# Performance work log

Hardware: AMD Instinct MI355X
Metric: run time of the kernel (lower is better)

Reference implementation:

```python
import jax, jax.numpy as jnp
import numpy as np


def setup_inputs() -> dict:
    key = jax.random.key(0)
    k0, k1, k2, k3 = jax.random.split(key, 4)
    B, T, D, F, E = 4, 2048, 512, 1024, 8
    x = jax.random.normal(k0, (B, T, D), dtype=jnp.float32)
    # router weight is zero-init in the original; use small random values so top-k
    router_w = 0.02 * jax.random.normal(k1, (E, D), dtype=jnp.float32)
    router_b = jnp.zeros((E,), dtype=jnp.float32)
    w_gate_up = 0.02 * jax.random.normal(k2, (E, D, 2 * F), dtype=jnp.float32)
    w_down = 0.02 * jax.random.normal(k3, (E, F, D), dtype=jnp.float32)
    return {"x": x, "router_w": router_w, "router_b": router_b,
            "w_gate_up": w_gate_up, "w_down": w_down, "top_k": 2}


def reference(x, router_w, router_b, w_gate_up, w_down, top_k):
    B, T, D = x.shape
    E = router_w.shape[0]
    x_flat = x.reshape(-1, D)                      # [N, D]
    N = x_flat.shape[0]

    # router: softmax over experts, top-k, renormalize
    logits = x_flat @ router_w.T + router_b       # [N, E]
    probs = jax.nn.softmax(logits, axis=-1)
    top_w, top_idx = jax.lax.top_k(probs, top_k)  # [N, k]
    top_w = top_w / jnp.sum(top_w, axis=-1, keepdims=True)

    # scatter renormalized weights into a dense [N, E] combine matrix
    combine = jnp.zeros((N, E), dtype=x.dtype).at[
        jnp.arange(N)[:, None], top_idx].add(top_w)

    # per-expert SwiGLU; combine weights zero out non-selected experts, giving
    # math identical to the sort/gather/scatter dispatch in the original
    out = jnp.zeros_like(x_flat)
    for e in range(E):  # fixed small expert count, not a data-dim loop
        gate_up = x_flat @ w_gate_up[e]           # [N, 2F]
        gate, up = jnp.split(gate_up, 2, axis=-1)
        h = jax.nn.silu(gate) * up                # [N, F]
        out = out + combine[:, e:e + 1] * (h @ w_down[e])
    return out.reshape(B, T, D)
```

## Files before the change

### kernel.cpp

```cpp
#include <hip/hip_runtime.h>
#include <stdint.h>

#define N_TOK 8192
#define D_DIM 512
#define F_DIM 1024
#define E_NUM 8
#define M_SLOTS (N_TOK * 2)

typedef __bf16 bf16x8 __attribute__((ext_vector_type(8)));
typedef float f32x4 __attribute__((ext_vector_type(4)));

__device__ __forceinline__ ushort f2b(float f) {
    union { float f; unsigned u; } v; v.f = f;
    unsigned r = v.u + 0x7fffu + ((v.u >> 16) & 1u);
    return (ushort)(r >> 16);
}
__device__ __forceinline__ float b2f(ushort u) {
    union { unsigned i; float f; } v; v.i = ((unsigned)u) << 16; return v.f;
}
__device__ __forceinline__ void gload16(const void* g, void* l) {
    __builtin_amdgcn_global_load_lds(
        (const __attribute__((address_space(1))) unsigned int*)g,
        (__attribute__((address_space(3))) unsigned int*)l, 16, 0, 0);
}

__global__ void init_k(int* cnt) {
    if (threadIdx.x < 16) cnt[threadIdx.x] = 0;
}

__global__ __launch_bounds__(256) void transpose_k(const float* __restrict__ in,
                                                   ushort* __restrict__ out,
                                                   int R, int C) {
    __shared__ ushort tile[64][66];
    int e = blockIdx.z;
    const float* src = in + (size_t)e * R * C;
    ushort* dst = out + (size_t)e * R * C;
    int c0 = blockIdx.x * 64, r0 = blockIdx.y * 64;
    for (int i = threadIdx.x; i < 64 * 64; i += 256) {
        int r = i >> 6, c = i & 63;
        tile[r][c] = f2b(src[(size_t)(r0 + r) * C + c0 + c]);
    }
    __syncthreads();
    for (int i = threadIdx.x; i < 64 * 64; i += 256) {
        int c = i >> 6, r = i & 63;
        dst[(size_t)(c0 + c) * R + r0 + r] = tile[r][c];
    }
}

__global__ __launch_bounds__(256) void logits_k(const float* __restrict__ x,
                                                const float* __restrict__ rw,
                                                const float* __restrict__ rb,
                                                ushort* __restrict__ x_bf,
                                                int* __restrict__ tok_e,
                                                float* __restrict__ tok_w) {
    int lane = threadIdx.x & 63, wv = threadIdx.x >> 6;
    int t = blockIdx.x * 4 + wv;
    float4 xa = *(const float4*)(x + (size_t)t * D_DIM + lane * 8);
    float4 xb = *(const float4*)(x + (size_t)t * D_DIM + lane * 8 + 4);
    ushort u[8] = {f2b(xa.x), f2b(xa.y), f2b(xa.z), f2b(xa.w),
                   f2b(xb.x), f2b(xb.y), f2b(xb.z), f2b(xb.w)};
    *(uint4*)(x_bf + (size_t)t * D_DIM + lane * 8) = *(const uint4*)u;

    float acc[E_NUM];
#pragma unroll
    for (int e = 0; e < E_NUM; ++e) {
        float4 wa = *(const float4*)(rw + (size_t)e * D_DIM + lane * 8);
        float4 wb = *(const float4*)(rw + (size_t)e * D_DIM + lane * 8 + 4);
        float s = xa.x * wa.x + xa.y * wa.y + xa.z * wa.z + xa.w * wa.w +
                  xb.x * wb.x + xb.y * wb.y + xb.z * wb.z + xb.w * wb.w;
#pragma unroll
        for (int o = 32; o > 0; o >>= 1) s += __shfl_xor(s, o, 64);
        acc[e] = s;
    }
    if (lane == 0) {
        float l[E_NUM];
#pragma unroll
        for (int e = 0; e < E_NUM; ++e) l[e] = acc[e] + rb[e];
        int e0 = 0;
#pragma unroll
        for (int e = 1; e < E_NUM; ++e) if (l[e] > l[e0]) e0 = e;
        int e1 = (e0 == 0) ? 1 : 0;
#pragma unroll
        for (int e = 0; e < E_NUM; ++e) if (e != e0 && l[e] > l[e1]) e1 = e;
        float p1 = __expf(l[e1] - l[e0]);
        float w0 = 1.f / (1.f + p1), w1 = p1 / (1.f + p1);
        tok_e[2 * t] = e0;  tok_e[2 * t + 1] = e1;
        tok_w[2 * t] = w0;  tok_w[2 * t + 1] = w1;
    }
}

__global__ __launch_bounds__(256) void assign_k(const int* __restrict__ tok_e,
                                                int* __restrict__ cnt,
                                                int* __restrict__ rank) {
    __shared__ int lcnt[E_NUM], lbase[E_NUM];
    int tid = threadIdx.x;
    int i = blockIdx.x * 256 + tid;
    if (tid < E_NUM) lcnt[tid] = 0;
    __syncthreads();
    int e = tok_e[i];
    int intra = atomicAdd(&lcnt[e], 1);
    __syncthreads();
    if (tid < E_NUM) lbase[tid] = atomicAdd(&cnt[tid], lcnt[tid]);
    __syncthreads();
    rank[i] = lbase[e] + intra;
}

__global__ void prefix_k(const int* __restrict__ cnt, int* __restrict__ ebase) {
    if (threadIdx.x == 0) {
        int s = 0;
        for (int e = 0; e < E_NUM; ++e) { ebase[e] = s; s += cnt[e]; }
        ebase[E_NUM] = s;
    }
}

__global__ __launch_bounds__(256) void scatter_k(const int* __restrict__ tok_e,
                                                 const int* __restrict__ rank,
                                                 const int* __restrict__ ebase,
                                                 int* __restrict__ row_token,
                                                 int* __restrict__ tok_pos) {
    int i = blockIdx.x * 256 + threadIdx.x;
    int pos = ebase[tok_e[i]] + rank[i];
    row_token[pos] = i >> 1;
    tok_pos[i] = pos;
}

__global__ __launch_bounds__(256, 4) void gemm1_k(const ushort* __restrict__ x,
                                                  const ushort* __restrict__ wgu_t,
                                                  const int* __restrict__ ebase,
                                                  const int* __restrict__ row_token,
                                                  ushort* __restrict__ h) {
    int e = blockIdx.z;
    int base = ebase[e];
    int cnt = ebase[e + 1] - base;
    int tile0 = blockIdx.y * 128;
    if (tile0 >= cnt) return;
    int c0 = blockIdx.x * 64;

    __shared__ ushort smem[128 * 32 + 128 * 32];
    ushort* lds_a = smem;
    ushort* lds_b = smem + 128 * 32;

    int tid = threadIdx.x;
    int lane = tid & 63, wv = tid >> 6;
    int wr = wv >> 1, wc = wv & 1;

    const ushort* asrc[2];
#pragma unroll
    for (int i = 0; i < 2; ++i) {
        int c = tid + i * 256;
        int r = tile0 + (c >> 2);
        r = (r < cnt) ? r : (cnt - 1);
        int tok = row_token[base + r];
        asrc[i] = x + (size_t)tok * D_DIM + (c & 3) * 8;
    }
    const ushort* bsrc[2];
#pragma unroll
    for (int i = 0; i < 2; ++i) {
        int c = tid + i * 256;
        int brow = c >> 2;
        int gc = (brow < 64) ? (c0 + brow) : (F_DIM + c0 + brow - 64);
        bsrc[i] = wgu_t + ((size_t)e * (2 * F_DIM) + gc) * D_DIM + (c & 3) * 8;
    }

    f32x4 accg[4][2], accu[4][2];
#pragma unroll
    for (int a = 0; a < 4; ++a)
#pragma unroll
        for (int b = 0; b < 2; ++b) {
            accg[a][b] = (f32x4){0.f, 0.f, 0.f, 0.f};
            accu[a][b] = (f32x4){0.f, 0.f, 0.f, 0.f};
        }

    for (int k0 = 0; k0 < D_DIM; k0 += 32) {
        __syncthreads();
#pragma unroll
        for (int i = 0; i < 2; ++i) {
            int c = tid + i * 256;
            gload16(asrc[i] + k0, lds_a + (size_t)c * 8);
            gload16(bsrc[i] + k0, lds_b + (size_t)c * 8);
        }
        __syncthreads();

        int q = lane >> 4, m = lane & 15;
        bf16x8 af[4], bg[2], bu[2];
#pragma unroll
        for (int mt = 0; mt < 4; ++mt)
            af[mt] = *(const bf16x8*)(lds_a + (wr * 64 + mt * 16 + m) * 32 + q * 8);
#pragma unroll
        for (int nt = 0; nt < 2; ++nt) {
            bg[nt] = *(const bf16x8*)(lds_b + (wc * 32 + nt * 16 + m) * 32 + q * 8);
            bu[nt] = *(const bf16x8*)(lds_b + (64 + wc * 32 + nt * 16 + m) * 32 + q * 8);
        }
#pragma unroll
        for (int mt = 0; mt < 4; ++mt)
#pragma unroll
            for (int nt = 0; nt < 2; ++nt) {
                accg[mt][nt] = __builtin_amdgcn_mfma_f32_16x16x32_bf16(af[mt], bg[nt], accg[mt][nt], 0, 0, 0);
                accu[mt][nt] = __builtin_amdgcn_mfma_f32_16x16x32_bf16(af[mt], bu[nt], accu[mt][nt], 0, 0, 0);
            }
    }

    ushort* stg = smem;
    int q = lane >> 4, col = lane & 15;
    __syncthreads();
#pragma unroll
    for (int mt = 0; mt < 4; ++mt) {
#pragma unroll
        for (int nt = 0; nt < 2; ++nt) {
            int sc = wc * 32 + nt * 16 + col;
#pragma unroll
            for (int r4 = 0; r4 < 4; ++r4) {
                int sr = wr * 16 + q * 4 + r4;
                float g = accg[mt][nt][r4];
                float u = accu[mt][nt][r4];
                stg[sr * 68 + sc] = f2b((g / (1.f + __expf(-g))) * u);
            }
        }
        __syncthreads();
        {
            int sr = tid >> 3;
            int coff = (tid & 7) * 8;
            int grow = tile0 + (sr >> 4) * 64 + mt * 16 + (sr & 15);
            if (grow < cnt)
                *(uint4*)(h + (size_t)(base + grow) * F_DIM + c0 + coff) =
                    *(const uint4*)(stg + sr * 68 + coff);
        }
        __syncthreads();
    }
}

__global__ __launch_bounds__(256, 4) void gemm2_k(const ushort* __restrict__ h,
                                                  const ushort* __restrict__ wd_t,
                                                  const int* __restrict__ ebase,
                                                  ushort* __restrict__ slot) {
    int e = blockIdx.z;
    int base = ebase[e];
    int cnt = ebase[e + 1] - base;
    int tile0 = blockIdx.y * 128;
    if (tile0 >= cnt) return;
    int c0 = blockIdx.x * 128;

    __shared__ ushort smem[128 * 32 + 128 * 32];
    ushort* lds_a = smem;
    ushort* lds_b = smem + 128 * 32;

    int tid = threadIdx.x;
    int lane = tid & 63, wv = tid >> 6;
    int wr = wv >> 1, wc = wv & 1;

    const ushort* asrc[2]; const ushort* bsrc[2];
#pragma unroll
    for (int i = 0; i < 2; ++i) {
        int c = tid + i * 256;
        int r = tile0 + (c >> 2);
        r = (r < cnt) ? r : (cnt - 1);
        asrc[i] = h + (size_t)(base + r) * F_DIM + (c & 3) * 8;
        int brow = c >> 2;
        bsrc[i] = wd_t + ((size_t)e * D_DIM + c0 + brow) * F_DIM + (c & 3) * 8;
    }

    f32x4 acc[4][4];
#pragma unroll
    for (int a = 0; a < 4; ++a)
#pragma unroll
        for (int b = 0; b < 4; ++b) acc[a][b] = (f32x4){0.f, 0.f, 0.f, 0.f};

    for (int k0 = 0; k0 < F_DIM; k0 += 32) {
        __syncthreads();
#pragma unroll
        for (int i = 0; i < 2; ++i) {
            int c = tid + i * 256;
            gload16(asrc[i] + k0, lds_a + (size_t)c * 8);
            gload16(bsrc[i] + k0, lds_b + (size_t)c * 8);
        }
        __syncthreads();

        int q = lane >> 4, m = lane & 15;
        bf16x8 af[4], bb[4];
#pragma unroll
        for (int mt = 0; mt < 4; ++mt)
            af[mt] = *(const bf16x8*)(lds_a + (wr * 64 + mt * 16 + m) * 32 + q * 8);
#pragma unroll
        for (int nt = 0; nt < 4; ++nt)
            bb[nt] = *(const bf16x8*)(lds_b + (wc * 64 + nt * 16 + m) * 32 + q * 8);
#pragma unroll
        for (int mt = 0; mt < 4; ++mt)
#pragma unroll
            for (int nt = 0; nt < 4; ++nt)
                acc[mt][nt] = __builtin_amdgcn_mfma_f32_16x16x32_bf16(af[mt], bb[nt], acc[mt][nt], 0, 0, 0);
    }

    ushort* stg = smem;
    int q = lane >> 4, col = lane & 15;
    __syncthreads();
#pragma unroll
    for (int mt = 0; mt < 4; ++mt) {
#pragma unroll
        for (int nt = 0; nt < 4; ++nt) {
            int scol = wc * 64 + nt * 16 + col;
#pragma unroll
            for (int r4 = 0; r4 < 4; ++r4) {
                int sr = wr * 16 + q * 4 + r4;
                stg[sr * 132 + scol] = f2b(acc[mt][nt][r4]);
            }
        }
        __syncthreads();
#pragma unroll
        for (int i = 0; i < 2; ++i) {
            int c = tid + i * 256;
            int sr = c >> 4;
            int coff = (c & 15) * 8;
            int grow = tile0 + (sr >> 4) * 64 + mt * 16 + (sr & 15);
            if (grow < cnt)
                *(uint4*)(slot + (size_t)(base + grow) * D_DIM + c0 + coff) =
                    *(const uint4*)(stg + sr * 132 + coff);
        }
        __syncthreads();
    }
}

__global__ __launch_bounds__(256) void combine_k(const ushort* __restrict__ slot,
                                                 const int* __restrict__ tok_pos,
                                                 const float* __restrict__ tok_w,
                                                 float* __restrict__ out) {
    int lane = threadIdx.x & 63, wv = threadIdx.x >> 6;
    int t = blockIdx.x * 4 + wv;
    int p0 = tok_pos[2 * t], p1 = tok_pos[2 * t + 1];
    float w0 = tok_w[2 * t], w1 = tok_w[2 * t + 1];
    uint4 s0 = *(const uint4*)(slot + (size_t)p0 * D_DIM + lane * 8);
    uint4 s1 = *(const uint4*)(slot + (size_t)p1 * D_DIM + lane * 8);
    const ushort* a = (const ushort*)&s0;
    const ushort* b = (const ushort*)&s1;
    float o[8];
#pragma unroll
    for (int j = 0; j < 8; ++j) o[j] = w0 * b2f(a[j]) + w1 * b2f(b[j]);
    float* dst = out + (size_t)t * D_DIM + lane * 8;
    *(float4*)dst = (float4){o[0], o[1], o[2], o[3]};
    *(float4*)(dst + 4) = (float4){o[4], o[5], o[6], o[7]};
}

extern "C" void kernel_launch(void* const* d_in, const int* in_sizes, int n_in,
                              void* d_out, int out_size, void* d_ws, size_t ws_size,
                              hipStream_t stream) {
    const float* x   = (const float*)d_in[0];
    const float* rw  = (const float*)d_in[1];
    const float* rb  = (const float*)d_in[2];
    const float* wgu = (const float*)d_in[3];
    const float* wd  = (const float*)d_in[4];
    float* out = (float*)d_out;

    char* ws = (char*)d_ws;
    size_t off = 0;
    auto alloc = [&](size_t bytes) -> void* {
        void* p = ws + off;
        off += (bytes + 255) & ~(size_t)255;
        return p;
    };
    ushort* wgu_t     = (ushort*)alloc((size_t)E_NUM * 2 * F_DIM * D_DIM * 2);
    ushort* wd_t      = (ushort*)alloc((size_t)E_NUM * D_DIM * F_DIM * 2);
    ushort* x_bf      = (ushort*)alloc((size_t)N_TOK * D_DIM * 2);
    ushort* hbuf      = (ushort*)alloc((size_t)M_SLOTS * F_DIM * 2);
    ushort* slot      = (ushort*)alloc((size_t)M_SLOTS * D_DIM * 2);
    int*    row_token = (int*)alloc(M_SLOTS * 4);
    int*    tok_e     = (int*)alloc(M_SLOTS * 4);
    int*    rankbuf   = (int*)alloc(M_SLOTS * 4);
    float*  tok_w     = (float*)alloc(M_SLOTS * 4);
    int*    tok_pos   = (int*)alloc(M_SLOTS * 4);
    int*    cnt       = (int*)alloc(64);
    int*    ebase     = (int*)alloc(64);

    init_k<<<1, 64, 0, stream>>>(cnt);
    transpose_k<<<dim3(2 * F_DIM / 64, D_DIM / 64, E_NUM), 256, 0, stream>>>(wgu, wgu_t, D_DIM, 2 * F_DIM);
    transpose_k<<<dim3(D_DIM / 64, F_DIM / 64, E_NUM), 256, 0, stream>>>(wd, wd_t, F_DIM, D_DIM);
    logits_k<<<N_TOK / 4, 256, 0, stream>>>(x, rw, rb, x_bf, tok_e, tok_w);
    assign_k<<<M_SLOTS / 256, 256, 0, stream>>>(tok_e, cnt, rankbuf);
    prefix_k<<<1, 64, 0, stream>>>(cnt, ebase);
    scatter_k<<<M_SLOTS / 256, 256, 0, stream>>>(tok_e, rankbuf, ebase, row_token, tok_pos);
    gemm1_k<<<dim3(16, 32, E_NUM), 256, 0, stream>>>(x_bf, wgu_t, ebase, row_token, hbuf);
    gemm2_k<<<dim3(4, 32, E_NUM), 256, 0, stream>>>(hbuf, wd_t, ebase, slot);
    combine_k<<<N_TOK / 4, 256, 0, stream>>>(slot, tok_pos, tok_w, out);
}
```

Measured before the change: 233.3 us.

## Double K-tile depth to 64 and XOR-swizzle LDS layout in both expert GEMMs

Both grouped GEMM kernels now stage 64-wide K slices per iteration instead of 32, which halves the number of barrier pairs and loop iterations. The LDS tiles use an XOR swizzle on the 16-byte chunk index (chunk ^ row&7), applied to the global source addresses so the direct-to-LDS loads land in swizzled positions. The fragment reads apply the same swizzle, which is meant to avoid bank conflicts that the wider 128-byte rows would otherwise cause. LDS per block doubles to 32 KB, which may reduce occupancy.

```diff
diff --git a/kernel.cpp b/kernel.cpp
--- a/kernel.cpp
+++ b/kernel.cpp
@@ -136,30 +136,33 @@
     if (tile0 >= cnt) return;
     int c0 = blockIdx.x * 64;
 
-    __shared__ ushort smem[128 * 32 + 128 * 32];
+    __shared__ ushort smem[128 * 64 + 128 * 64];
     ushort* lds_a = smem;
-    ushort* lds_b = smem + 128 * 32;
+    ushort* lds_b = smem + 128 * 64;
 
     int tid = threadIdx.x;
     int lane = tid & 63, wv = tid >> 6;
     int wr = wv >> 1, wc = wv & 1;
 
-    const ushort* asrc[2];
-#pragma unroll
-    for (int i = 0; i < 2; ++i) {
+    const ushort* asrc[4];
+#pragma unroll
+    for (int i = 0; i < 4; ++i) {
         int c = tid + i * 256;
-        int r = tile0 + (c >> 2);
+        int row = c >> 3;
+        int r = tile0 + row;
         r = (r < cnt) ? r : (cnt - 1);
         int tok = row_token[base + r];
-        asrc[i] = x + (size_t)tok * D_DIM + (c & 3) * 8;
-    }
-    const ushort* bsrc[2];
-#pragma unroll
-    for (int i = 0; i < 2; ++i) {
+        int qq = (c & 7) ^ (row & 7);
+        asrc[i] = x + (size_t)tok * D_DIM + qq * 8;
+    }
+    const ushort* bsrc[4];
+#pragma unroll
+    for (int i = 0; i < 4; ++i) {
         int c = tid + i * 256;
-        int brow = c >> 2;
+        int brow = c >> 3;
         int gc = (brow < 64) ? (c0 + brow) : (F_DIM + c0 + brow - 64);
-        bsrc[i] = wgu_t + ((size_t)e * (2 * F_DIM) + gc) * D_DIM + (c & 3) * 8;
+        int qq = (c & 7) ^ (brow & 7);
+        bsrc[i] = wgu_t + ((size_t)e * (2 * F_DIM) + gc) * D_DIM + qq * 8;
     }
 
     f32x4 accg[4][2], accu[4][2];
@@ -171,10 +174,10 @@
             accu[a][b] = (f32x4){0.f, 0.f, 0.f, 0.f};
         }
 
-    for (int k0 = 0; k0 < D_DIM; k0 += 32) {
-        __syncthreads();
-#pragma unroll
-        for (int i = 0; i < 2; ++i) {
+    for (int k0 = 0; k0 < D_DIM; k0 += 64) {
+        __syncthreads();
+#pragma unroll
+        for (int i = 0; i < 4; ++i) {
             int c = tid + i * 256;
             gload16(asrc[i] + k0, lds_a + (size_t)c * 8);
             gload16(bsrc[i] + k0, lds_b + (size_t)c * 8);
@@ -182,22 +185,31 @@
         __syncthreads();
 
         int q = lane >> 4, m = lane & 15;
-        bf16x8 af[4], bg[2], bu[2];
-#pragma unroll
-        for (int mt = 0; mt < 4; ++mt)
-            af[mt] = *(const bf16x8*)(lds_a + (wr * 64 + mt * 16 + m) * 32 + q * 8);
-#pragma unroll
-        for (int nt = 0; nt < 2; ++nt) {
-            bg[nt] = *(const bf16x8*)(lds_b + (wc * 32 + nt * 16 + m) * 32 + q * 8);
-            bu[nt] = *(const bf16x8*)(lds_b + (64 + wc * 32 + nt * 16 + m) * 32 + q * 8);
-        }
-#pragma unroll
-        for (int mt = 0; mt < 4; ++mt)
+#pragma unroll
+        for (int s = 0; s < 2; ++s) {
+            bf16x8 af[4], bg[2], bu[2];
+#pragma unroll
+            for (int mt = 0; mt < 4; ++mt) {
+                int row = wr * 64 + mt * 16 + m;
+                int qq = s * 4 + q;
+                af[mt] = *(const bf16x8*)(lds_a + row * 64 + (qq ^ (row & 7)) * 8);
+            }
 #pragma unroll
             for (int nt = 0; nt < 2; ++nt) {
-                accg[mt][nt] = __builtin_amdgcn_mfma_f32_16x16x32_bf16(af[mt], bg[nt], accg[mt][nt], 0, 0, 0);
-                accu[mt][nt] = __builtin_amdgcn_mfma_f32_16x16x32_bf16(af[mt], bu[nt], accu[mt][nt], 0, 0, 0);
-            }
+                int rg = wc * 32 + nt * 16 + m;
+                int ru = 64 + rg;
+                int qq = s * 4 + q;
+                bg[nt] = *(const bf16x8*)(lds_b + rg * 64 + (qq ^ (rg & 7)) * 8);
+                bu[nt] = *(const bf16x8*)(lds_b + ru * 64 + (qq ^ (ru & 7)) * 8);
+            }
+#pragma unroll
+            for (int mt = 0; mt < 4; ++mt)
+#pragma unroll
+                for (int nt = 0; nt < 2; ++nt) {
+                    accg[mt][nt] = __builtin_amdgcn_mfma_f32_16x16x32_bf16(af[mt], bg[nt], accg[mt][nt], 0, 0, 0);
+                    accu[mt][nt] = __builtin_amdgcn_mfma_f32_16x16x32_bf16(af[mt], bu[nt], accu[mt][nt], 0, 0, 0);
+                }
+        }
     }
 
     ushort* stg = smem;
@@ -240,23 +252,24 @@
     if (tile0 >= cnt) return;
     int c0 = blockIdx.x * 128;
 
-    __shared__ ushort smem[128 * 32 + 128 * 32];
+    __shared__ ushort smem[128 * 64 + 128 * 64];
     ushort* lds_a = smem;
-    ushort* lds_b = smem + 128 * 32;
+    ushort* lds_b = smem + 128 * 64;
 
     int tid = threadIdx.x;
     int lane = tid & 63, wv = tid >> 6;
     int wr = wv >> 1, wc = wv & 1;
 
-    const ushort* asrc[2]; const ushort* bsrc[2];
-#pragma unroll
-    for (int i = 0; i < 2; ++i) {
+    const ushort* asrc[4]; const ushort* bsrc[4];
+#pragma unroll
+    for (int i = 0; i < 4; ++i) {
         int c = tid + i * 256;
-        int r = tile0 + (c >> 2);
+        int row = c >> 3;
+        int r = tile0 + row;
         r = (r < cnt) ? r : (cnt - 1);
-        asrc[i] = h + (size_t)(base + r) * F_DIM + (c & 3) * 8;
-        int brow = c >> 2;
-        bsrc[i] = wd_t + ((size_t)e * D_DIM + c0 + brow) * F_DIM + (c & 3) * 8;
+        int qq = (c & 7) ^ (row & 7);
+        asrc[i] = h + (size_t)(base + r) * F_DIM + qq * 8;
+        bsrc[i] = wd_t + ((size_t)e * D_DIM + c0 + row) * F_DIM + qq * 8;
     }
 
     f32x4 acc[4][4];
@@ -265,10 +278,10 @@
 #pragma unroll
         for (int b = 0; b < 4; ++b) acc[a][b] = (f32x4){0.f, 0.f, 0.f, 0.f};
 
-    for (int k0 = 0; k0 < F_DIM; k0 += 32) {
-        __syncthreads();
-#pragma unroll
-        for (int i = 0; i < 2; ++i) {
+    for (int k0 = 0; k0 < F_DIM; k0 += 64) {
+        __syncthreads();
+#pragma unroll
+        for (int i = 0; i < 4; ++i) {
             int c = tid + i * 256;
             gload16(asrc[i] + k0, lds_a + (size_t)c * 8);
             gload16(bsrc[i] + k0, lds_b + (size_t)c * 8);
@@ -276,18 +289,27 @@
         __syncthreads();
 
         int q = lane >> 4, m = lane & 15;
-        bf16x8 af[4], bb[4];
-#pragma unroll
-        for (int mt = 0; mt < 4; ++mt)
-            af[mt] = *(const bf16x8*)(lds_a + (wr * 64 + mt * 16 + m) * 32 + q * 8);
-#pragma unroll
-        for (int nt = 0; nt < 4; ++nt)
-            bb[nt] = *(const bf16x8*)(lds_b + (wc * 64 + nt * 16 + m) * 32 + q * 8);
-#pragma unroll
-        for (int mt = 0; mt < 4; ++mt)
-#pragma unroll
-            for (int nt = 0; nt < 4; ++nt)
-                acc[mt][nt] = __builtin_amdgcn_mfma_f32_16x16x32_bf16(af[mt], bb[nt], acc[mt][nt], 0, 0, 0);
+#pragma unroll
+        for (int s = 0; s < 2; ++s) {
+            bf16x8 af[4], bb[4];
+#pragma unroll
+            for (int mt = 0; mt < 4; ++mt) {
+                int row = wr * 64 + mt * 16 + m;
+                int qq = s * 4 + q;
+                af[mt] = *(const bf16x8*)(lds_a + row * 64 + (qq ^ (row & 7)) * 8);
+            }
+#pragma unroll
+            for (int nt = 0; nt < 4; ++nt) {
+                int row = wc * 64 + nt * 16 + m;
+                int qq = s * 4 + q;
+                bb[nt] = *(const bf16x8*)(lds_b + row * 64 + (qq ^ (row & 7)) * 8);
+            }
+#pragma unroll
+            for (int mt = 0; mt < 4; ++mt)
+#pragma unroll
+                for (int nt = 0; nt < 4; ++nt)
+                    acc[mt][nt] = __builtin_amdgcn_mfma_f32_16x16x32_bf16(af[mt], bb[nt], acc[mt][nt], 0, 0, 0);
+        }
     }
 
     ushort* stg = smem;
```

Measured after the change: 273.3 us. +17.1%, slower.
